# Optimization experiments

Hardware: AMD Instinct MI355X
Metric: run time of the kernel (lower is better)

## Reference

```python
import jax, jax.numpy as jnp
import numpy as np

D = 4  # max_displacement

def setup_inputs() -> dict:
    key = jax.random.key(0)
    k1, k2 = jax.random.split(key)
    fa = jax.random.normal(k1, (8, 256, 96, 128), dtype=jnp.float32)
    fb = jax.random.normal(k2, (8, 256, 96, 128), dtype=jnp.float32)
    return {"fa": fa, "fb": fb}

def _l2_normalize(x):
    # matches torch F.normalize(p=2, dim=1, eps=1e-12)
    n = jnp.sqrt(jnp.sum(x * x, axis=1, keepdims=True))
    return x / jnp.maximum(n, 1e-12)

def reference(fa, fb):
    B, C, H, W = fa.shape
    d = D
    fa = _l2_normalize(fa)
    fb = _l2_normalize(fb)
    fbp = jnp.pad(fb, ((0, 0), (0, 0), (d, d), (d, d)))
    # fixed small loop over (2d+1)^2 = 81 shifts; each dot is (B,H,W)
    corr = [
        jnp.sum(fa * jax.lax.dynamic_slice(fbp, (0, 0, dy, dx), (B, C, H, W)), axis=1)
        for dy in range(2 * d + 1)
        for dx in range(2 * d + 1)
    ]
    return jnp.stack(corr, axis=1)  # (B, (2d+1)^2, H, W)
```

## Files before the change

### kernel.cpp

```cpp
#include <hip/hip_runtime.h>
#include <math.h>

namespace {
constexpr int Bn = 8, Cn = 256, Hn = 96, Wn = 128;
constexpr int HWn = Hn * Wn;
constexpr int CHWn = Cn * HWn;
constexpr int Kn = 81;
constexpr int TW = 32, TH = 8;
constexpr int HR = TH + 8;
constexpr int HC = TW + 8;
constexpr int HCP = 44;
constexpr int CC = 8;
constexpr int NTHREADS = 8 * 3 * 8;
}

__global__ __launch_bounds__(NTHREADS)
void corr81_kernel(const float* __restrict__ fa,
                   const float* __restrict__ fb,
                   float* __restrict__ out) {
  __shared__ __align__(16) float lfb[CC][HR][HCP];
  __shared__ float ssb[HR * HC];

  const int tx = threadIdx.x;
  const int g  = threadIdx.y;
  const int ty = threadIdx.z;
  const int tid = tx + 8 * g + 24 * ty;

  const int flat = blockIdx.x;
  const int o = (flat & 7) * 48 + (flat >> 3);
  const int b  = o / 48;
  const int r  = o % 48;
  const int h0 = (r >> 2) * TH;
  const int w0 = (r & 3) * TW;
  const int wb = w0 + 4 * tx;

  for (int i = tid; i < HR * HC; i += NTHREADS) ssb[i] = 0.0f;

  float acc[27][4];
  #pragma unroll
  for (int k = 0; k < 27; ++k) {
    #pragma unroll
    for (int j = 0; j < 4; ++j) acc[k][j] = 0.0f;
  }
  float ssa[4] = {0.f, 0.f, 0.f, 0.f};

  const float* faP = fa + (size_t)b * CHWn + (h0 + ty) * Wn + wb;

  int   s_hr[4], s_hc[4];
  bool  s_on[4], s_ok[4];
  const float* s_ptr[4];
  #pragma unroll
  for (int i = 0; i < 4; ++i) {
    int px = tid + NTHREADS * i;
    s_on[i] = (px < HR * HC);
    int hr = px / HC, hc = px - hr * HC;
    s_hr[i] = hr; s_hc[i] = hc;
    int gh = h0 - 4 + hr, gw = w0 - 4 + hc;
    s_ok[i] = s_on[i] && gh >= 0 && gh < Hn && gw >= 0 && gw < Wn;
    s_ptr[i] = fb + (size_t)b * CHWn + (size_t)gh * Wn + gw;
  }
  __syncthreads();

  for (int c0 = 0; c0 < Cn; c0 += CC) {
    #pragma unroll
    for (int i = 0; i < 4; ++i) {
      if (s_on[i]) {
        float ss = 0.f;
        if (s_ok[i]) {
          const float* p = s_ptr[i] + (size_t)c0 * HWn;
          #pragma unroll
          for (int cc = 0; cc < CC; ++cc) {
            float v = p[(size_t)cc * HWn];
            lfb[cc][s_hr[i]][s_hc[i]] = v;
            ss += v * v;
          }
        } else {
          #pragma unroll
          for (int cc = 0; cc < CC; ++cc) lfb[cc][s_hr[i]][s_hc[i]] = 0.f;
        }
        ssb[s_hr[i] * HC + s_hc[i]] += ss;
      }
    }
    float4 areg[CC];
    #pragma unroll
    for (int cc = 0; cc < CC; ++cc)
      areg[cc] = *(const float4*)(faP + (size_t)(c0 + cc) * HWn);
    __syncthreads();

    #pragma unroll
    for (int cc = 0; cc < CC; ++cc) {
      const float a0 = areg[cc].x, a1 = areg[cc].y, a2 = areg[cc].z, a3 = areg[cc].w;
      ssa[0] += a0 * a0; ssa[1] += a1 * a1; ssa[2] += a2 * a2; ssa[3] += a3 * a3;
      #pragma unroll
      for (int ro = 0; ro < 3; ++ro) {
        const float* rowp = &lfb[cc][ty + 3 * g + ro][4 * tx];
        const float4 wa = *(const float4*)(rowp);
        const float4 wv = *(const float4*)(rowp + 4);
        const float4 wc = *(const float4*)(rowp + 8);
        const float win[12] = {wa.x, wa.y, wa.z, wa.w,
                               wv.x, wv.y, wv.z, wv.w,
                               wc.x, wc.y, wc.z, wc.w};
        #pragma unroll
        for (int dx = 0; dx < 9; ++dx) {
          acc[ro * 9 + dx][0] += a0 * win[dx + 0];
          acc[ro * 9 + dx][1] += a1 * win[dx + 1];
          acc[ro * 9 + dx][2] += a2 * win[dx + 2];
          acc[ro * 9 + dx][3] += a3 * win[dx + 3];
        }
      }
    }
    __syncthreads();
  }

  for (int i = tid; i < HR * HC; i += NTHREADS) {
    ssb[i] = 1.0f / fmaxf(sqrtf(ssb[i]), 1e-12f);
  }
  float rna[4];
  #pragma unroll
  for (int j = 0; j < 4; ++j) rna[j] = 1.0f / fmaxf(sqrtf(ssa[j]), 1e-12f);
  __syncthreads();

  float* outP = out + (size_t)b * (Kn * HWn) + (h0 + ty) * Wn + wb;
  #pragma unroll
  for (int ro = 0; ro < 3; ++ro) {
    const int dy = 3 * g + ro;
    const int rr = ty + dy;
    #pragma unroll
    for (int dx = 0; dx < 9; ++dx) {
      const int k = dy * 9 + dx;
      float4 v;
      v.x = acc[ro * 9 + dx][0] * rna[0] * ssb[rr * HC + 4 * tx + dx + 0];
      v.y = acc[ro * 9 + dx][1] * rna[1] * ssb[rr * HC + 4 * tx + dx + 1];
      v.z = acc[ro * 9 + dx][2] * rna[2] * ssb[rr * HC + 4 * tx + dx + 2];
      v.w = acc[ro * 9 + dx][3] * rna[3] * ssb[rr * HC + 4 * tx + dx + 3];
      *(float4*)(outP + (size_t)k * HWn) = v;
    }
  }
}

extern "C" void kernel_launch(void* const* d_in, const int* in_sizes, int n_in,
                              void* d_out, int out_size, void* d_ws, size_t ws_size,
                              hipStream_t stream) {
  const float* fa = (const float*)d_in[0];
  const float* fb = (const float*)d_in[1];
  float* outp = (float*)d_out;
  dim3 grid(Bn * 48);
  dim3 block(8, 3, 8);
  hipLaunchKernelGGL(corr81_kernel, grid, block, 0, stream, fa, fb, outp);
}
```

Measured before the change: 329.1 us.

## Shrink per-thread dy work to one row and tile height to six

Each thread now computes a single dy row of nine displacements instead of three, with block dims grown to 8x9x6 (432 threads) and tile height cut from 8 to 6 rows, giving 512 blocks. Accumulator registers drop from 108 to 36 floats, and launch bounds request 4 blocks per SM, to raise occupancy and block count across CUs. In exchange, each fa value is loaded by nine threads instead of three, and the halo-to-tile ratio for fb staging grows, increasing global and LDS traffic per output.

```diff
diff --git a/kernel.cpp b/kernel.cpp
--- a/kernel.cpp
+++ b/kernel.cpp
@@ -6,39 +6,40 @@
 constexpr int HWn = Hn * Wn;
 constexpr int CHWn = Cn * HWn;
 constexpr int Kn = 81;
-constexpr int TW = 32, TH = 8;
+constexpr int TW = 32, TH = 6;
 constexpr int HR = TH + 8;
 constexpr int HC = TW + 8;
 constexpr int HCP = 44;
 constexpr int CC = 8;
-constexpr int NTHREADS = 8 * 3 * 8;
+constexpr int NTHREADS = 8 * 9 * 6;
+constexpr int HALO = HR * HC;
 }
 
-__global__ __launch_bounds__(NTHREADS)
+__global__ __launch_bounds__(NTHREADS, 4)
 void corr81_kernel(const float* __restrict__ fa,
                    const float* __restrict__ fb,
                    float* __restrict__ out) {
   __shared__ __align__(16) float lfb[CC][HR][HCP];
-  __shared__ float ssb[HR * HC];
+  __shared__ float ssb[HALO];
 
   const int tx = threadIdx.x;
   const int g  = threadIdx.y;
   const int ty = threadIdx.z;
-  const int tid = tx + 8 * g + 24 * ty;
+  const int tid = tx + 8 * g + 72 * ty;
 
   const int flat = blockIdx.x;
-  const int o = (flat & 7) * 48 + (flat >> 3);
-  const int b  = o / 48;
-  const int r  = o % 48;
+  const int o = (flat & 7) * 64 + (flat >> 3);
+  const int b  = o >> 6;
+  const int r  = o & 63;
   const int h0 = (r >> 2) * TH;
   const int w0 = (r & 3) * TW;
   const int wb = w0 + 4 * tx;
 
-  for (int i = tid; i < HR * HC; i += NTHREADS) ssb[i] = 0.0f;
+  for (int i = tid; i < HALO; i += NTHREADS) ssb[i] = 0.0f;
 
-  float acc[27][4];
+  float acc[9][4];
   #pragma unroll
-  for (int k = 0; k < 27; ++k) {
+  for (int k = 0; k < 9; ++k) {
     #pragma unroll
     for (int j = 0; j < 4; ++j) acc[k][j] = 0.0f;
   }
@@ -46,13 +47,13 @@
 
   const float* faP = fa + (size_t)b * CHWn + (h0 + ty) * Wn + wb;
 
-  int   s_hr[4], s_hc[4];
-  bool  s_on[4], s_ok[4];
-  const float* s_ptr[4];
+  int   s_hr[2], s_hc[2];
+  bool  s_on[2], s_ok[2];
+  const float* s_ptr[2];
   #pragma unroll
-  for (int i = 0; i < 4; ++i) {
+  for (int i = 0; i < 2; ++i) {
     int px = tid + NTHREADS * i;
-    s_on[i] = (px < HR * HC);
+    s_on[i] = (px < HALO);
     int hr = px / HC, hc = px - hr * HC;
     s_hr[i] = hr; s_hc[i] = hc;
     int gh = h0 - 4 + hr, gw = w0 - 4 + hc;
@@ -63,7 +64,7 @@
 
   for (int c0 = 0; c0 < Cn; c0 += CC) {
     #pragma unroll
-    for (int i = 0; i < 4; ++i) {
+    for (int i = 0; i < 2; ++i) {
       if (s_on[i]) {
         float ss = 0.f;
         if (s_ok[i]) {
@@ -91,28 +92,25 @@
     for (int cc = 0; cc < CC; ++cc) {
       const float a0 = areg[cc].x, a1 = areg[cc].y, a2 = areg[cc].z, a3 = areg[cc].w;
       ssa[0] += a0 * a0; ssa[1] += a1 * a1; ssa[2] += a2 * a2; ssa[3] += a3 * a3;
+      const float* rowp = &lfb[cc][ty + g][4 * tx];
+      const float4 wa = *(const float4*)(rowp);
+      const float4 wv = *(const float4*)(rowp + 4);
+      const float4 wc = *(const float4*)(rowp + 8);
+      const float win[12] = {wa.x, wa.y, wa.z, wa.w,
+                             wv.x, wv.y, wv.z, wv.w,
+                             wc.x, wc.y, wc.z, wc.w};
       #pragma unroll
-      for (int ro = 0; ro < 3; ++ro) {
-        const float* rowp = &lfb[cc][ty + 3 * g + ro][4 * tx];
-        const float4 wa = *(const float4*)(rowp);
-        const float4 wv = *(const float4*)(rowp + 4);
-        const float4 wc = *(const float4*)(rowp + 8);
-        const float win[12] = {wa.x, wa.y, wa.z, wa.w,
-                               wv.x, wv.y, wv.z, wv.w,
-                               wc.x, wc.y, wc.z, wc.w};
-        #pragma unroll
-        for (int dx = 0; dx < 9; ++dx) {
-          acc[ro * 9 + dx][0] += a0 * win[dx + 0];
-          acc[ro * 9 + dx][1] += a1 * win[dx + 1];
-          acc[ro * 9 + dx][2] += a2 * win[dx + 2];
-          acc[ro * 9 + dx][3] += a3 * win[dx + 3];
-        }
+      for (int dx = 0; dx < 9; ++dx) {
+        acc[dx][0] += a0 * win[dx + 0];
+        acc[dx][1] += a1 * win[dx + 1];
+        acc[dx][2] += a2 * win[dx + 2];
+        acc[dx][3] += a3 * win[dx + 3];
       }
     }
     __syncthreads();
   }
 
-  for (int i = tid; i < HR * HC; i += NTHREADS) {
+  for (int i = tid; i < HALO; i += NTHREADS) {
     ssb[i] = 1.0f / fmaxf(sqrtf(ssb[i]), 1e-12f);
   }
   float rna[4];
@@ -121,20 +119,16 @@
   __syncthreads();
 
   float* outP = out + (size_t)b * (Kn * HWn) + (h0 + ty) * Wn + wb;
+  const int rr = ty + g;
   #pragma unroll
-  for (int ro = 0; ro < 3; ++ro) {
-    const int dy = 3 * g + ro;
-    const int rr = ty + dy;
-    #pragma unroll
-    for (int dx = 0; dx < 9; ++dx) {
-      const int k = dy * 9 + dx;
-      float4 v;
-      v.x = acc[ro * 9 + dx][0] * rna[0] * ssb[rr * HC + 4 * tx + dx + 0];
-      v.y = acc[ro * 9 + dx][1] * rna[1] * ssb[rr * HC + 4 * tx + dx + 1];
-      v.z = acc[ro * 9 + dx][2] * rna[2] * ssb[rr * HC + 4 * tx + dx + 2];
-      v.w = acc[ro * 9 + dx][3] * rna[3] * ssb[rr * HC + 4 * tx + dx + 3];
-      *(float4*)(outP + (size_t)k * HWn) = v;
-    }
+  for (int dx = 0; dx < 9; ++dx) {
+    const int k = g * 9 + dx;
+    float4 v;
+    v.x = acc[dx][0] * rna[0] * ssb[rr * HC + 4 * tx + dx + 0];
+    v.y = acc[dx][1] * rna[1] * ssb[rr * HC + 4 * tx + dx + 1];
+    v.z = acc[dx][2] * rna[2] * ssb[rr * HC + 4 * tx + dx + 2];
+    v.w = acc[dx][3] * rna[3] * ssb[rr * HC + 4 * tx + dx + 3];
+    *(float4*)(outP + (size_t)k * HWn) = v;
   }
 }
 
@@ -144,7 +138,7 @@
   const float* fa = (const float*)d_in[0];
   const float* fb = (const float*)d_in[1];
   float* outp = (float*)d_out;
-  dim3 grid(Bn * 48);
-  dim3 block(8, 3, 8);
+  dim3 grid(512);
+  dim3 block(8, 9, 6);
   hipLaunchKernelGGL(corr81_kernel, grid, block, 0, stream, fa, fb, outp);
 }
```

New measurement: 275.7 us. 1.19x faster.
